# Performance work log

Measured on AMD Instinct MI355X. Metric: run time of the kernel, lower is better.

## Reference

```python
import jax, jax.numpy as jnp
import numpy as np

EPS = 1e-6  # torch F.pairwise_distance default eps added to the difference


def setup_inputs() -> dict:
    key = jax.random.key(0)
    k1, k2 = jax.random.split(key)
    N, D = 8192, 256
    embeddings = jax.random.normal(k1, (N, D), dtype=jnp.float32)
    labels = jax.random.randint(k2, (N,), 0, 64, dtype=jnp.int32)
    return {"embeddings": embeddings, "labels": labels}


def reference(embeddings, labels):
    # Fused replacement for the O(N^2) python loop:
    # dist[i,j] = ||e_i - e_j + EPS||_2 (torch pairwise_distance semantics)
    #           = sqrt(||e_i||^2 + ||e_j||^2 - 2 e_i.e_j + 2*EPS*(sum(e_i)-sum(e_j)) + D*EPS^2)
    N, D = embeddings.shape
    sq_norm = jnp.sum(embeddings * embeddings, axis=-1)        # (N,)
    row_sum = jnp.sum(embeddings, axis=-1)                     # (N,)
    gram = embeddings @ embeddings.T                           # (N, N)
    sq = (sq_norm[:, None] + sq_norm[None, :] - 2.0 * gram
          + 2.0 * EPS * (row_sum[:, None] - row_sum[None, :])
          + D * EPS * EPS)
    dist = jnp.sqrt(jnp.maximum(sq, 0.0))                      # (N, N)
    mask = labels[:, None] == labels[None, :]                  # (N, N) bool
    loss = jnp.sum(jnp.where(mask, dist, 0.0)) / (N * (N - 1))
    return loss
```

## Files before the change

kernel.cpp:

```cpp
#include <hip/hip_runtime.h>
#include <stdint.h>


#define NROWS 8192
#define DDIM 256
#define NLAB 64
#define NBLK (NLAB * 4)

typedef __attribute__((ext_vector_type(8))) short bfrag8;
typedef __attribute__((ext_vector_type(4))) float f32x4;

__device__ __forceinline__ unsigned short f2bf(float f) {
  unsigned u = __float_as_uint(f);
  u += 0x7FFFu + ((u >> 16) & 1u);
  return (unsigned short)(u >> 16);
}

__global__ void __launch_bounds__(512)
k_fused(const float* __restrict__ E, const int* __restrict__ lab,
        float* __restrict__ partials) {
  __shared__ __align__(16) char As[128 * 512];
  __shared__ __align__(16) char Bs[128 * 512];
  __shared__ int rowlistS[256];
  __shared__ float qAS[128], qBS[128];
  __shared__ int wcntS[8];
  __shared__ float wsum[8];

  const int bid = blockIdx.x;
  const int g = bid >> 2, p = bid & 3;
  const int t = threadIdx.x, l = t & 63, w = t >> 6;
  const bool diag = (p < 2);
  const int a0 = (p == 1) ? 128 : ((p == 3) ? 64 : 0);
  const int b0 = (p == 0) ? 0 : 128;

  int lv[16];
  #pragma unroll
  for (int i = 0; i < 16; ++i)
    lv[i] = lab[(w * 16 + i) * 64 + l];

  int cntw = 0;
  #pragma unroll
  for (int i = 0; i < 16; ++i)
    cntw += (int)__popcll(__ballot(lv[i] == g));
  if (l == 0) wcntS[w] = cntw;
  if (t == 0) rowlistS[0] = 0;
  __syncthreads();
  int n_total = 0, base = 0;
  #pragma unroll
  for (int w2 = 0; w2 < 8; ++w2) {
    const int c = wcntS[w2];
    n_total += c;
    base += (w2 < w) ? c : 0;
  }
  #pragma unroll
  for (int i = 0; i < 16; ++i) {
    const unsigned long long m = __ballot(lv[i] == g);
    if (lv[i] == g) {
      const int rank = base + (int)__popcll(m & ((1ull << l) - 1ull));
      if (rank < 256) rowlistS[rank] = (w * 16 + i) * 64 + l;
    }
    base += (int)__popcll(m);
  }
  const int n = min(n_total, 256);
  __syncthreads();

  float blocksum = 0.f;
  const bool active = (a0 < n) && (b0 < n);
  if (active) {
    const int gsw = l >> 1;
    const int half8 = (l & 1) * 8;
    if (diag) {
      #pragma unroll 8
      for (int r8 = 0; r8 < 16; ++r8) {
        const int r = w * 16 + r8;
        const int gi = a0 + r;
        const int grow = rowlistS[(gi < n) ? gi : 0];
        const float4 v = *reinterpret_cast<const float4*>(E + (size_t)grow * DDIM + l * 4);
        ushort4 b4;
        b4.x = f2bf(v.x); b4.y = f2bf(v.y); b4.z = f2bf(v.z); b4.w = f2bf(v.w);
        *reinterpret_cast<ushort4*>(
            As + r * 512 + ((gsw ^ (r & 15)) << 4) + half8) = b4;
      }
    } else {
      #pragma unroll 8
      for (int r8 = 0; r8 < 16; ++r8) {
        const int rB = w * 16 + r8;
        const int gj = 128 + rB;
        const int growB = rowlistS[(gj < n) ? gj : 0];
        const float4 vb = *reinterpret_cast<const float4*>(E + (size_t)growB * DDIM + l * 4);
        if (r8 < 8) {
          const int rA = w * 8 + r8;
          const int gi = a0 + rA;
          const int growA = rowlistS[(gi < n) ? gi : 0];
          const float4 va = *reinterpret_cast<const float4*>(E + (size_t)growA * DDIM + l * 4);
          ushort4 ba;
          ba.x = f2bf(va.x); ba.y = f2bf(va.y); ba.z = f2bf(va.z); ba.w = f2bf(va.w);
          *reinterpret_cast<ushort4*>(
              As + rA * 512 + ((gsw ^ (rA & 15)) << 4) + half8) = ba;
        }
        ushort4 bb;
        bb.x = f2bf(vb.x); bb.y = f2bf(vb.y); bb.z = f2bf(vb.z); bb.w = f2bf(vb.w);
        *reinterpret_cast<ushort4*>(
            Bs + rB * 512 + ((gsw ^ (rB & 15)) << 4) + half8) = bb;
      }
    }
    __syncthreads();

    if (diag) {
      const int r = t >> 2, q4 = t & 3;
      float q = 0.f;
      #pragma unroll
      for (int i = 0; i < 8; ++i) {
        const int gidx = q4 * 8 + i;
        const bfrag8 v = *reinterpret_cast<const bfrag8*>(
            As + r * 512 + ((gidx ^ (r & 15)) << 4));
        #pragma unroll
        for (int e = 0; e < 8; ++e) {
          const float f = __uint_as_float(((unsigned)(unsigned short)v[e]) << 16);
          q = fmaf(f, f, q);
        }
      }
      q += __shfl_xor(q, 1);
      q += __shfl_xor(q, 2);
      if ((t & 3) == 0) qAS[r] = q;
    } else {
      const int rAll = t >> 1, hf = t & 1;
      if (rAll < 192) {
        const bool isA = rAll < 64;
        const int r = isA ? rAll : rAll - 64;
        const char* buf = isA ? As : Bs;
        float q = 0.f;
        #pragma unroll
        for (int i = 0; i < 16; ++i) {
          const int gidx = hf * 16 + i;
          const bfrag8 v = *reinterpret_cast<const bfrag8*>(
              buf + r * 512 + ((gidx ^ (r & 15)) << 4));
          #pragma unroll
          for (int e = 0; e < 8; ++e) {
            const float f = __uint_as_float(((unsigned)(unsigned short)v[e]) << 16);
            q = fmaf(f, f, q);
          }
        }
        q += __shfl_xor(q, 1);
        if (hf == 0) { if (isA) qAS[r] = q; else qBS[r] = q; }
      }
    }

    const int colsel = l & 15;
    const int ksel = l >> 4;
    const int wr = w >> 2, wc = w & 3;
    float lsum = 0.f;

    if (diag) {
      f32x4 acc[4][2];
      const f32x4 zero = {0.f, 0.f, 0.f, 0.f};
      #pragma unroll
      for (int m = 0; m < 4; ++m)
        #pragma unroll
        for (int nn = 0; nn < 2; ++nn)
          acc[m][nn] = zero;
      #pragma unroll
      for (int kk = 0; kk < 8; ++kk) {
        bfrag8 af[4], bf[2];
        #pragma unroll
        for (int m = 0; m < 4; ++m) {
          const int row = wr * 64 + m * 16 + colsel;
          const int gidx = (kk * 4 + ksel) ^ (row & 15);
          af[m] = *reinterpret_cast<const bfrag8*>(As + row * 512 + (gidx << 4));
        }
        #pragma unroll
        for (int nn = 0; nn < 2; ++nn) {
          const int row = wc * 32 + nn * 16 + colsel;
          const int gidx = (kk * 4 + ksel) ^ (row & 15);
          bf[nn] = *reinterpret_cast<const bfrag8*>(As + row * 512 + (gidx << 4));
        }
        #pragma unroll
        for (int m = 0; m < 4; ++m)
          #pragma unroll
          for (int nn = 0; nn < 2; ++nn)
            acc[m][nn] = __builtin_amdgcn_mfma_f32_16x16x32_bf16(af[m], bf[nn],
                                                                 acc[m][nn], 0, 0, 0);
      }
      __syncthreads();
      #pragma unroll
      for (int m = 0; m < 4; ++m) {
        const int ib = wr * 64 + m * 16 + ksel * 4;
        const int gi = a0 + ib;
        const float q0 = qAS[ib], q1 = qAS[ib + 1], q2 = qAS[ib + 2], q3 = qAS[ib + 3];
        #pragma unroll
        for (int nn = 0; nn < 2; ++nn) {
          const int jb = wc * 32 + nn * 16 + colsel;
          const int gj = a0 + jb;
          const bool jv = gj < n;
          const float qj = qAS[jb];
          const f32x4 a = acc[m][nn];
          const float d0 = __builtin_amdgcn_sqrtf(fmaxf(q0 + qj - 2.f * a[0], 0.f));
          const float d1 = __builtin_amdgcn_sqrtf(fmaxf(q1 + qj - 2.f * a[1], 0.f));
          const float d2 = __builtin_amdgcn_sqrtf(fmaxf(q2 + qj - 2.f * a[2], 0.f));
          const float d3 = __builtin_amdgcn_sqrtf(fmaxf(q3 + qj - 2.f * a[3], 0.f));
          if (jv) {
            lsum += (gi + 0 < n && gi + 0 != gj) ? d0 : 0.f;
            lsum += (gi + 1 < n && gi + 1 != gj) ? d1 : 0.f;
            lsum += (gi + 2 < n && gi + 2 != gj) ? d2 : 0.f;
            lsum += (gi + 3 < n && gi + 3 != gj) ? d3 : 0.f;
          }
        }
      }
    } else {
      f32x4 acc[2][2];
      const f32x4 zero = {0.f, 0.f, 0.f, 0.f};
      #pragma unroll
      for (int m = 0; m < 2; ++m)
        #pragma unroll
        for (int nn = 0; nn < 2; ++nn)
          acc[m][nn] = zero;
      #pragma unroll
      for (int kk = 0; kk < 8; ++kk) {
        bfrag8 af[2], bf[2];
        #pragma unroll
        for (int m = 0; m < 2; ++m) {
          const int row = wr * 32 + m * 16 + colsel;
          const int gidx = (kk * 4 + ksel) ^ (row & 15);
          af[m] = *reinterpret_cast<const bfrag8*>(As + row * 512 + (gidx << 4));
        }
        #pragma unroll
        for (int nn = 0; nn < 2; ++nn) {
          const int row = wc * 32 + nn * 16 + colsel;
          const int gidx = (kk * 4 + ksel) ^ (row & 15);
          bf[nn] = *reinterpret_cast<const bfrag8*>(Bs + row * 512 + (gidx << 4));
        }
        #pragma unroll
        for (int m = 0; m < 2; ++m)
          #pragma unroll
          for (int nn = 0; nn < 2; ++nn)
            acc[m][nn] = __builtin_amdgcn_mfma_f32_16x16x32_bf16(af[m], bf[nn],
                                                                 acc[m][nn], 0, 0, 0);
      }
      __syncthreads();
      #pragma unroll
      for (int m = 0; m < 2; ++m) {
        const int ib = wr * 32 + m * 16 + ksel * 4;
        const int gi = a0 + ib;
        const float q0 = qAS[ib], q1 = qAS[ib + 1], q2 = qAS[ib + 2], q3 = qAS[ib + 3];
        #pragma unroll
        for (int nn = 0; nn < 2; ++nn) {
          const int jb = wc * 32 + nn * 16 + colsel;
          const int gj = 128 + jb;
          const bool jv = gj < n;
          const float qj = qBS[jb];
          const f32x4 a = acc[m][nn];
          const float d0 = __builtin_amdgcn_sqrtf(fmaxf(q0 + qj - 2.f * a[0], 0.f));
          const float d1 = __builtin_amdgcn_sqrtf(fmaxf(q1 + qj - 2.f * a[1], 0.f));
          const float d2 = __builtin_amdgcn_sqrtf(fmaxf(q2 + qj - 2.f * a[2], 0.f));
          const float d3 = __builtin_amdgcn_sqrtf(fmaxf(q3 + qj - 2.f * a[3], 0.f));
          if (jv) {
            lsum += (gi + 0 < n) ? d0 : 0.f;
            lsum += (gi + 1 < n) ? d1 : 0.f;
            lsum += (gi + 2 < n) ? d2 : 0.f;
            lsum += (gi + 3 < n) ? d3 : 0.f;
          }
        }
      }
      lsum *= 2.0f;
    }

    #pragma unroll
    for (int o = 32; o; o >>= 1) lsum += __shfl_down(lsum, o);
    if (l == 0) wsum[w] = lsum;
    __syncthreads();
    blocksum = wsum[0] + wsum[1] + wsum[2] + wsum[3] +
               wsum[4] + wsum[5] + wsum[6] + wsum[7];
  }

  if (t == 0) partials[bid] = blocksum;
}

__global__ void __launch_bounds__(64)
k_final(const float* __restrict__ partials, float* __restrict__ out, double invn) {
  const int l = threadIdx.x;
  double s = (double)partials[l] + (double)partials[l + 64] +
             (double)partials[l + 128] + (double)partials[l + 192];
  #pragma unroll
  for (int o = 32; o; o >>= 1) s += __shfl_down(s, o);
  if (l == 0) out[0] = (float)(s * invn);
}

extern "C" void kernel_launch(void* const* d_in, const int* in_sizes, int n_in,
                              void* d_out, int out_size, void* d_ws, size_t ws_size,
                              hipStream_t stream) {
  const float* E = (const float*)d_in[0];
  const int* lab = (const int*)d_in[1];
  float* out = (float*)d_out;
  (void)n_in; (void)in_sizes; (void)out_size; (void)ws_size;

  float* partials = (float*)d_ws;

  const double invn = 1.0 / ((double)NROWS * (double)(NROWS - 1));
  k_fused<<<NBLK, 512, 0, stream>>>(E, lab, partials);
  k_final<<<1, 64, 0, stream>>>(partials, out, invn);
}
```

Measured before the change: 15.33 us.

## Split off-diagonal tile staging so half the warps compute while others load

In off-diagonal blocks only the first 64 rows of the B tile are staged before the first barrier. Warps whose columns need the second half of B prefetch those rows into registers, compute row norms, then convert and write them to shared memory. Meanwhile the other warps run their MFMA loop, and a second phase swaps the roles. The aim is to overlap global loads of the B tile with matrix-core work, at the cost of an extra barrier, more register pressure from the 16-element float4 prefetch, and less even work across warps.

```diff
diff --git a/kernel.cpp b/kernel.cpp
--- a/kernel.cpp
+++ b/kernel.cpp
@@ -69,6 +69,11 @@
   if (active) {
     const int gsw = l >> 1;
     const int half8 = (l & 1) * 8;
+    const int colsel = l & 15;
+    const int ksel = l >> 4;
+    const int wr = w >> 2, wc = w & 3;
+    float lsum = 0.f;
+
     if (diag) {
       #pragma unroll 8
       for (int r8 = 0; r8 < 16; ++r8) {
@@ -81,60 +86,16 @@
         *reinterpret_cast<ushort4*>(
             As + r * 512 + ((gsw ^ (r & 15)) << 4) + half8) = b4;
       }
-    } else {
-      #pragma unroll 8
-      for (int r8 = 0; r8 < 16; ++r8) {
-        const int rB = w * 16 + r8;
-        const int gj = 128 + rB;
-        const int growB = rowlistS[(gj < n) ? gj : 0];
-        const float4 vb = *reinterpret_cast<const float4*>(E + (size_t)growB * DDIM + l * 4);
-        if (r8 < 8) {
-          const int rA = w * 8 + r8;
-          const int gi = a0 + rA;
-          const int growA = rowlistS[(gi < n) ? gi : 0];
-          const float4 va = *reinterpret_cast<const float4*>(E + (size_t)growA * DDIM + l * 4);
-          ushort4 ba;
-          ba.x = f2bf(va.x); ba.y = f2bf(va.y); ba.z = f2bf(va.z); ba.w = f2bf(va.w);
-          *reinterpret_cast<ushort4*>(
-              As + rA * 512 + ((gsw ^ (rA & 15)) << 4) + half8) = ba;
-        }
-        ushort4 bb;
-        bb.x = f2bf(vb.x); bb.y = f2bf(vb.y); bb.z = f2bf(vb.z); bb.w = f2bf(vb.w);
-        *reinterpret_cast<ushort4*>(
-            Bs + rB * 512 + ((gsw ^ (rB & 15)) << 4) + half8) = bb;
-      }
-    }
-    __syncthreads();
-
-    if (diag) {
-      const int r = t >> 2, q4 = t & 3;
-      float q = 0.f;
-      #pragma unroll
-      for (int i = 0; i < 8; ++i) {
-        const int gidx = q4 * 8 + i;
-        const bfrag8 v = *reinterpret_cast<const bfrag8*>(
-            As + r * 512 + ((gidx ^ (r & 15)) << 4));
-        #pragma unroll
-        for (int e = 0; e < 8; ++e) {
-          const float f = __uint_as_float(((unsigned)(unsigned short)v[e]) << 16);
-          q = fmaf(f, f, q);
-        }
-      }
-      q += __shfl_xor(q, 1);
-      q += __shfl_xor(q, 2);
-      if ((t & 3) == 0) qAS[r] = q;
-    } else {
-      const int rAll = t >> 1, hf = t & 1;
-      if (rAll < 192) {
-        const bool isA = rAll < 64;
-        const int r = isA ? rAll : rAll - 64;
-        const char* buf = isA ? As : Bs;
+      __syncthreads();
+
+      {
+        const int r = t >> 2, q4 = t & 3;
         float q = 0.f;
         #pragma unroll
-        for (int i = 0; i < 16; ++i) {
-          const int gidx = hf * 16 + i;
+        for (int i = 0; i < 8; ++i) {
+          const int gidx = q4 * 8 + i;
           const bfrag8 v = *reinterpret_cast<const bfrag8*>(
-              buf + r * 512 + ((gidx ^ (r & 15)) << 4));
+              As + r * 512 + ((gidx ^ (r & 15)) << 4));
           #pragma unroll
           for (int e = 0; e < 8; ++e) {
             const float f = __uint_as_float(((unsigned)(unsigned short)v[e]) << 16);
@@ -142,16 +103,10 @@
           }
         }
         q += __shfl_xor(q, 1);
-        if (hf == 0) { if (isA) qAS[r] = q; else qBS[r] = q; }
-      }
-    }
-
-    const int colsel = l & 15;
-    const int ksel = l >> 4;
-    const int wr = w >> 2, wc = w & 3;
-    float lsum = 0.f;
-
-    if (diag) {
+        q += __shfl_xor(q, 2);
+        if ((t & 3) == 0) qAS[r] = q;
+      }
+
       f32x4 acc[4][2];
       const f32x4 zero = {0.f, 0.f, 0.f, 0.f};
       #pragma unroll
@@ -182,6 +137,7 @@
                                                                  acc[m][nn], 0, 0, 0);
       }
       __syncthreads();
+
       #pragma unroll
       for (int m = 0; m < 4; ++m) {
         const int ib = wr * 64 + m * 16 + ksel * 4;
@@ -207,6 +163,26 @@
         }
       }
     } else {
+      #pragma unroll 8
+      for (int r8 = 0; r8 < 8; ++r8) {
+        const int rA = w * 8 + r8;
+        const int rB = w * 8 + r8;
+        const int gi = a0 + rA;
+        const int gj = 128 + rB;
+        const int growA = rowlistS[(gi < n) ? gi : 0];
+        const int growB = rowlistS[(gj < n) ? gj : 0];
+        const float4 va = *reinterpret_cast<const float4*>(E + (size_t)growA * DDIM + l * 4);
+        const float4 vb = *reinterpret_cast<const float4*>(E + (size_t)growB * DDIM + l * 4);
+        ushort4 ba, bb;
+        ba.x = f2bf(va.x); ba.y = f2bf(va.y); ba.z = f2bf(va.z); ba.w = f2bf(va.w);
+        bb.x = f2bf(vb.x); bb.y = f2bf(vb.y); bb.z = f2bf(vb.z); bb.w = f2bf(vb.w);
+        *reinterpret_cast<ushort4*>(
+            As + rA * 512 + ((gsw ^ (rA & 15)) << 4) + half8) = ba;
+        *reinterpret_cast<ushort4*>(
+            Bs + rB * 512 + ((gsw ^ (rB & 15)) << 4) + half8) = bb;
+      }
+      __syncthreads();
+
       f32x4 acc[2][2];
       const f32x4 zero = {0.f, 0.f, 0.f, 0.f};
       #pragma unroll
@@ -214,29 +190,137 @@
         #pragma unroll
         for (int nn = 0; nn < 2; ++nn)
           acc[m][nn] = zero;
-      #pragma unroll
-      for (int kk = 0; kk < 8; ++kk) {
-        bfrag8 af[2], bf[2];
-        #pragma unroll
-        for (int m = 0; m < 2; ++m) {
-          const int row = wr * 32 + m * 16 + colsel;
-          const int gidx = (kk * 4 + ksel) ^ (row & 15);
-          af[m] = *reinterpret_cast<const bfrag8*>(As + row * 512 + (gidx << 4));
-        }
-        #pragma unroll
-        for (int nn = 0; nn < 2; ++nn) {
-          const int row = wc * 32 + nn * 16 + colsel;
-          const int gidx = (kk * 4 + ksel) ^ (row & 15);
-          bf[nn] = *reinterpret_cast<const bfrag8*>(Bs + row * 512 + (gidx << 4));
-        }
-        #pragma unroll
-        for (int m = 0; m < 2; ++m)
-          #pragma unroll
-          for (int nn = 0; nn < 2; ++nn)
-            acc[m][nn] = __builtin_amdgcn_mfma_f32_16x16x32_bf16(af[m], bf[nn],
-                                                                 acc[m][nn], 0, 0, 0);
-      }
-      __syncthreads();
+
+      if (wc >= 2) {
+        const int wHi = wr * 2 + (wc - 2);
+        float4 vb[16];
+        #pragma unroll
+        for (int r8 = 0; r8 < 16; ++r8) {
+          const int r = 64 + wHi * 16 + r8;
+          const int gj = 128 + r;
+          const int grow = rowlistS[(gj < n) ? gj : 0];
+          vb[r8] = *reinterpret_cast<const float4*>(E + (size_t)grow * DDIM + l * 4);
+        }
+        {
+          const int r = t >> 2, q4 = t & 3;
+          const char* buf = (r < 64) ? As : Bs;
+          const int rr = (r < 64) ? r : r - 64;
+          float q = 0.f;
+          #pragma unroll
+          for (int i = 0; i < 8; ++i) {
+            const int gidx = q4 * 8 + i;
+            const bfrag8 v = *reinterpret_cast<const bfrag8*>(
+                buf + rr * 512 + ((gidx ^ (rr & 15)) << 4));
+            #pragma unroll
+            for (int e = 0; e < 8; ++e) {
+              const float f = __uint_as_float(((unsigned)(unsigned short)v[e]) << 16);
+              q = fmaf(f, f, q);
+            }
+          }
+          q += __shfl_xor(q, 1);
+          q += __shfl_xor(q, 2);
+          if ((t & 3) == 0) { if (r < 64) qAS[r] = q; else qBS[r - 64] = q; }
+        }
+        #pragma unroll
+        for (int r8 = 0; r8 < 16; ++r8) {
+          const int r = 64 + wHi * 16 + r8;
+          ushort4 b4;
+          b4.x = f2bf(vb[r8].x); b4.y = f2bf(vb[r8].y);
+          b4.z = f2bf(vb[r8].z); b4.w = f2bf(vb[r8].w);
+          *reinterpret_cast<ushort4*>(
+              Bs + r * 512 + ((gsw ^ (r & 15)) << 4) + half8) = b4;
+        }
+      } else {
+        {
+          const int r = t >> 2, q4 = t & 3;
+          const char* buf = (r < 64) ? As : Bs;
+          const int rr = (r < 64) ? r : r - 64;
+          float q = 0.f;
+          #pragma unroll
+          for (int i = 0; i < 8; ++i) {
+            const int gidx = q4 * 8 + i;
+            const bfrag8 v = *reinterpret_cast<const bfrag8*>(
+                buf + rr * 512 + ((gidx ^ (rr & 15)) << 4));
+            #pragma unroll
+            for (int e = 0; e < 8; ++e) {
+              const float f = __uint_as_float(((unsigned)(unsigned short)v[e]) << 16);
+              q = fmaf(f, f, q);
+            }
+          }
+          q += __shfl_xor(q, 1);
+          q += __shfl_xor(q, 2);
+          if ((t & 3) == 0) { if (r < 64) qAS[r] = q; else qBS[r - 64] = q; }
+        }
+        #pragma unroll
+        for (int kk = 0; kk < 8; ++kk) {
+          bfrag8 af[2], bf[2];
+          #pragma unroll
+          for (int m = 0; m < 2; ++m) {
+            const int row = wr * 32 + m * 16 + colsel;
+            const int gidx = (kk * 4 + ksel) ^ (row & 15);
+            af[m] = *reinterpret_cast<const bfrag8*>(As + row * 512 + (gidx << 4));
+          }
+          #pragma unroll
+          for (int nn = 0; nn < 2; ++nn) {
+            const int row = wc * 32 + nn * 16 + colsel;
+            const int gidx = (kk * 4 + ksel) ^ (row & 15);
+            bf[nn] = *reinterpret_cast<const bfrag8*>(Bs + row * 512 + (gidx << 4));
+          }
+          #pragma unroll
+          for (int m = 0; m < 2; ++m)
+            #pragma unroll
+            for (int nn = 0; nn < 2; ++nn)
+              acc[m][nn] = __builtin_amdgcn_mfma_f32_16x16x32_bf16(af[m], bf[nn],
+                                                                   acc[m][nn], 0, 0, 0);
+        }
+      }
+      __syncthreads();
+
+      if (wc >= 2) {
+        #pragma unroll
+        for (int kk = 0; kk < 8; ++kk) {
+          bfrag8 af[2], bf[2];
+          #pragma unroll
+          for (int m = 0; m < 2; ++m) {
+            const int row = wr * 32 + m * 16 + colsel;
+            const int gidx = (kk * 4 + ksel) ^ (row & 15);
+            af[m] = *reinterpret_cast<const bfrag8*>(As + row * 512 + (gidx << 4));
+          }
+          #pragma unroll
+          for (int nn = 0; nn < 2; ++nn) {
+            const int row = wc * 32 + nn * 16 + colsel;
+            const int gidx = (kk * 4 + ksel) ^ (row & 15);
+            bf[nn] = *reinterpret_cast<const bfrag8*>(Bs + row * 512 + (gidx << 4));
+          }
+          #pragma unroll
+          for (int m = 0; m < 2; ++m)
+            #pragma unroll
+            for (int nn = 0; nn < 2; ++nn)
+              acc[m][nn] = __builtin_amdgcn_mfma_f32_16x16x32_bf16(af[m], bf[nn],
+                                                                   acc[m][nn], 0, 0, 0);
+        }
+      } else {
+        const int wLo = wr * 2 + wc;
+        const int tl = wLo * 64 + l;
+        const int r = 64 + (tl >> 2), q4 = tl & 3;
+        float q = 0.f;
+        #pragma unroll
+        for (int i = 0; i < 8; ++i) {
+          const int gidx = q4 * 8 + i;
+          const bfrag8 v = *reinterpret_cast<const bfrag8*>(
+              Bs + r * 512 + ((gidx ^ (r & 15)) << 4));
+          #pragma unroll
+          for (int e = 0; e < 8; ++e) {
+            const float f = __uint_as_float(((unsigned)(unsigned short)v[e]) << 16);
+            q = fmaf(f, f, q);
+          }
+        }
+        q += __shfl_xor(q, 1);
+        q += __shfl_xor(q, 2);
+        if ((tl & 3) == 0) qBS[r] = q;
+      }
+      __syncthreads();
+
       #pragma unroll
       for (int m = 0; m < 2; ++m) {
         const int ib = wr * 32 + m * 16 + ksel * 4;
```

Result: no change. 15.37 us (+0.2%).
